# Kernel tuning notes

Measured on AMD Instinct MI355X. Metric: run time of the kernel, lower is better.

## Reference

```python
import jax, jax.numpy as jnp
import numpy as np

B, N, EMB, H, C = 1, 4096, 256, 4, 64  # heads*C == 256 feeds Linear(256, EMB)
NEG_SLOPE = 0.2
LN_EPS = 1e-5


def setup_inputs() -> dict:
    key = jax.random.key(0)
    ks = jax.random.split(key, 8)
    x = jax.random.normal(ks[0], (B, N, EMB), jnp.float32)
    adj = jax.random.randint(ks[1], (B, N, N), 0, 2, jnp.int32)
    W_lin = jax.random.normal(ks[2], (EMB, H * C), jnp.float32) * (1.0 / EMB) ** 0.5
    att_src = jax.random.normal(ks[3], (H, C), jnp.float32) * 0.1
    att_dst = jax.random.normal(ks[4], (H, C), jnp.float32) * 0.1
    bias_att = jax.random.normal(ks[5], (H * C,), jnp.float32) * 0.02
    W_out = jax.random.normal(ks[6], (H * C, EMB), jnp.float32) * (1.0 / (H * C)) ** 0.5
    b_out = jax.random.normal(ks[7], (EMB,), jnp.float32) * 0.02
    gamma = jnp.ones((EMB,), jnp.float32)
    beta = jnp.zeros((EMB,), jnp.float32)
    return dict(x=x, adj=adj, W_lin=W_lin, att_src=att_src, att_dst=att_dst,
                bias_att=bias_att, W_out=W_out, b_out=b_out, gamma=gamma, beta=beta)


def reference(x, adj, W_lin, att_src, att_dst, bias_att, W_out, b_out, gamma, beta):
    # DenseGATConv (concat=True, add_loop=True, negative_slope=0.2)
    h = (x @ W_lin).reshape(B, N, H, C)                       # [B,N,H,C]
    a_src = jnp.einsum('bnhc,hc->bnh', h, att_src)            # per source node j
    a_dst = jnp.einsum('bnhc,hc->bnh', h, att_dst)            # per dest node i
    # alpha[b,i,j,h] = a_src[b,j,h] + a_dst[b,i,h]
    alpha = a_src[:, None, :, :] + a_dst[:, :, None, :]       # [B,N,N,H]
    alpha = jnp.where(alpha >= 0, alpha, NEG_SLOPE * alpha)   # leaky_relu
    # add self-loops to adjacency, then mask and softmax over source axis j
    idx = jnp.arange(N)
    adj_sl = adj.at[:, idx, idx].set(1)
    alpha = jnp.where(adj_sl[..., None] == 0, -jnp.inf, alpha)
    alpha = jax.nn.softmax(alpha, axis=2)                     # [B,N,N,H]
    out = jnp.einsum('bijh,bjhc->bihc', alpha, h)             # aggregate sources
    out = out.reshape(B, N, H * C) + bias_att                 # concat heads + GAT bias
    # trailing Linear + LayerNorm
    y = out @ W_out + b_out                                   # [B,N,EMB]
    mu = jnp.mean(y, axis=-1, keepdims=True)
    var = jnp.mean((y - mu) ** 2, axis=-1, keepdims=True)
    return (y - mu) * jax.lax.rsqrt(var + LN_EPS) * gamma + beta
```

## Files before the change

kernel.cpp:

```cpp
#include <hip/hip_runtime.h>
#include <stdint.h>

#define N    4096
#define EMB  256
#define NH   4
#define HC   64
#define PAD  40

typedef __attribute__((ext_vector_type(8))) short s16x8;
typedef __attribute__((ext_vector_type(4))) short s16x4;
typedef __attribute__((ext_vector_type(4))) float f32x4;
typedef __attribute__((ext_vector_type(4))) int   i32x4;
typedef unsigned short ushort_t;

__device__ __forceinline__ unsigned short f2bf(float f) {
  unsigned int u = __builtin_bit_cast(unsigned int, f);
  u += 0x7fffu + ((u >> 16) & 1u);
  return (unsigned short)(u >> 16);
}

__global__ __launch_bounds__(256)
void k_prep(const float* __restrict__ W0, ushort_t* __restrict__ WP0,
            const float* __restrict__ W1, ushort_t* __restrict__ WP1,
            const int* __restrict__ adj, unsigned int* __restrict__ abits)
{
  int b = blockIdx.x;
  if (b < 4096) {
    const int i = b;
    const int t = threadIdx.x;
    const int* src = adj + (size_t)i * N + t * 16;
    i32x4 v0 = *(const i32x4*)(src);
    i32x4 v1 = *(const i32x4*)(src + 4);
    i32x4 v2 = *(const i32x4*)(src + 8);
    i32x4 v3 = *(const i32x4*)(src + 12);
    unsigned int m = 0;
    #pragma unroll
    for (int u = 0; u < 4; ++u) {
      m |= (v0[u] != 0 ? 1u : 0u) << u;
      m |= (v1[u] != 0 ? 1u : 0u) << (4 + u);
      m |= (v2[u] != 0 ? 1u : 0u) << (8 + u);
      m |= (v3[u] != 0 ? 1u : 0u) << (12 + u);
    }
    if ((i >> 4) == t) m |= 1u << (i & 15);
    unsigned int partner = __shfl_xor(m, 1);
    if ((t & 1) == 0) {
      unsigned int word = m | (partner << 16);
      abits[(size_t)(t >> 1) * N + i] = word;
    }
  } else {
    b -= 4096;
    int k = b & 255;
    int m = threadIdx.x;
    size_t dst = ((size_t)(k >> 5) * 256 + m) * 32 + (k & 31);
    if (b < 256) WP0[dst] = f2bf(W0[k * EMB + m]);
    else         WP1[dst] = f2bf(W1[k * EMB + m]);
  }
}

__global__ __launch_bounds__(256, 2)
void k1_gemm_h(const float* __restrict__ x,
               const ushort_t* __restrict__ WlP,
               const float* __restrict__ att_src,
               const float* __restrict__ att_dst,
               ushort_t* __restrict__ hS,
               float* __restrict__ a_srcT,
               float* __restrict__ a_dstT)
{
  __shared__ ushort_t T_lds[64][PAD];
  __shared__ float red_lds[2][2][32];
  const int t = threadIdx.x;
  const int lane = t & 63;
  const int w = t >> 6;
  const int ihalf = w & 1, chalf = w >> 1;
  const int i0 = blockIdx.x * 32;
  const int head = blockIdx.y;
  const int c0 = head * 64;
  const int lq = lane >> 4, lm = lane & 15;

  f32x4 acc[2];
  acc[0] = f32x4{0.f, 0.f, 0.f, 0.f};
  acc[1] = f32x4{0.f, 0.f, 0.f, 0.f};

  const float* xrow = x + (size_t)(i0 + ihalf * 16 + lm) * EMB + lq * 8;
  const ushort_t* wp0 = WlP + (size_t)(c0 + chalf * 32 + lm) * 32 + lq * 8;
  const ushort_t* wp1 = WlP + (size_t)(c0 + chalf * 32 + 16 + lm) * 32 + lq * 8;

  #pragma unroll 2
  for (int kp = 0; kp < 8; ++kp) {
    f32x4 v0 = *(const f32x4*)(xrow + kp * 32);
    f32x4 v1 = *(const f32x4*)(xrow + kp * 32 + 4);
    s16x8 a;
    a[0]=(short)f2bf(v0[0]); a[1]=(short)f2bf(v0[1]); a[2]=(short)f2bf(v0[2]); a[3]=(short)f2bf(v0[3]);
    a[4]=(short)f2bf(v1[0]); a[5]=(short)f2bf(v1[1]); a[6]=(short)f2bf(v1[2]); a[7]=(short)f2bf(v1[3]);
    s16x8 b0 = *(const s16x8*)(wp0 + (size_t)kp * 8192);
    s16x8 b1 = *(const s16x8*)(wp1 + (size_t)kp * 8192);
    acc[0] = __builtin_amdgcn_mfma_f32_16x16x32_bf16(a, b0, acc[0], 0, 0, 0);
    acc[1] = __builtin_amdgcn_mfma_f32_16x16x32_bf16(a, b1, acc[1], 0, 0, 0);
  }

  float ps[4] = {0.f,0.f,0.f,0.f}, pd[4] = {0.f,0.f,0.f,0.f};
  #pragma unroll
  for (int nf = 0; nf < 2; ++nf) {
    int c = chalf * 32 + nf * 16 + lm;
    float wsv = att_src[c0 + c];
    float wdv = att_dst[c0 + c];
    #pragma unroll
    for (int r = 0; r < 4; ++r) {
      float v = acc[nf][r];
      T_lds[c][ihalf * 16 + lq * 4 + r] = f2bf(v);
      ps[r] += v * wsv;
      pd[r] += v * wdv;
    }
  }
  #pragma unroll
  for (int r = 0; r < 4; ++r) {
    #pragma unroll
    for (int mm = 1; mm < 16; mm <<= 1) {
      ps[r] += __shfl_xor(ps[r], mm);
      pd[r] += __shfl_xor(pd[r], mm);
    }
  }
  if (lm == 0) {
    #pragma unroll
    for (int r = 0; r < 4; ++r) {
      int node = ihalf * 16 + lq * 4 + r;
      red_lds[0][chalf][node] = ps[r];
      red_lds[1][chalf][node] = pd[r];
    }
  }
  __syncthreads();
  if (t < 32) {
    a_srcT[head * N + i0 + t] = red_lds[0][0][t] + red_lds[0][1][t];
    a_dstT[head * N + i0 + t] = red_lds[1][0][t] + red_lds[1][1][t];
  }
  {
    int c = t >> 2, seg = t & 3;
    s16x8 v = *(const s16x8*)&T_lds[c][seg * 8];
    size_t base = (((size_t)head * 128 + (i0 >> 5)) * 64 + c) * 32 + seg * 8;
    *(s16x8*)(hS + base) = v;
  }
}

__global__ __launch_bounds__(512, 1)
void k34_attn(const unsigned int* __restrict__ abits,
              const ushort_t* __restrict__ hS,
              const float* __restrict__ a_srcT,
              const float* __restrict__ a_dstT,
              const float* __restrict__ bias_att,
              ushort_t* __restrict__ oS)
{
  __shared__ float acc_lds[2][3][32][65];
  __shared__ float l_lds[2][4][32];

  const int t = threadIdx.x;
  const int lane = t & 63;
  const int w = t >> 6;
  const int hloc = w & 1;
  const int jq = w >> 1;
  const int head = blockIdx.y * 2 + hloc;
  const int i0 = blockIdx.x * 32;
  const int lm = lane & 15, lq = lane >> 4;
  const int ig0 = i0 + lm;
  const int ig1 = i0 + 16 + lm;

  const float* asrc_h = a_srcT + head * N;
  const ushort_t* hS_h = hS + (size_t)head * 128 * 64 * 32;
  const float ad0 = a_dstT[head * N + ig0];
  const float ad1 = a_dstT[head * N + ig1];

  f32x4 acc[2][4];
  #pragma unroll
  for (int s = 0; s < 2; ++s)
    #pragma unroll
    for (int nf = 0; nf < 4; ++nf) acc[s][nf] = f32x4{0.f, 0.f, 0.f, 0.f};
  float lp0 = 0.f, lp1 = 0.f;

  #pragma unroll 2
  for (int it = 0; it < 32; ++it) {
    const int jw = jq * 32 + it;
    const int jl = jw * 32 + lq * 8;

    unsigned int word0 = abits[(size_t)jw * N + ig0];
    unsigned int word1 = abits[(size_t)jw * N + ig1];
    f32x4 as0 = *(const f32x4*)(asrc_h + jl);
    f32x4 as1 = *(const f32x4*)(asrc_h + jl + 4);

    const ushort_t* tile = hS_h + (size_t)jw * 2048;
    s16x8 b0 = *(const s16x8*)(tile + ( 0 + lm) * 32 + lq * 8);
    s16x8 b1 = *(const s16x8*)(tile + (16 + lm) * 32 + lq * 8);
    s16x8 b2 = *(const s16x8*)(tile + (32 + lm) * 32 + lq * 8);
    s16x8 b3 = *(const s16x8*)(tile + (48 + lm) * 32 + lq * 8);

    unsigned int e0[8], e1[8];
    #pragma unroll
    for (int jj = 0; jj < 8; ++jj) {
      float asv = (jj < 4) ? as0[jj] : as1[jj - 4];
      float sc0 = asv + ad0;
      float sc1 = asv + ad1;
      sc0 = fmaxf(sc0, 0.2f * sc0);
      sc1 = fmaxf(sc1, 0.2f * sc1);
      bool c0 = (word0 >> (lq * 8 + jj)) & 1u;
      bool c1 = (word1 >> (lq * 8 + jj)) & 1u;
      float v0 = c0 ? __expf(sc0) : 0.f;
      float v1 = c1 ? __expf(sc1) : 0.f;
      unsigned int eb0 = __builtin_bit_cast(unsigned int, v0) & 0xffff0000u;
      unsigned int eb1 = __builtin_bit_cast(unsigned int, v1) & 0xffff0000u;
      e0[jj] = eb0;
      e1[jj] = eb1;
      lp0 += __builtin_bit_cast(float, eb0);
      lp1 += __builtin_bit_cast(float, eb1);
    }
    i32x4 p0, p1;
    #pragma unroll
    for (int u = 0; u < 4; ++u) {
      p0[u] = (int)__builtin_amdgcn_perm(e0[2 * u + 1], e0[2 * u], 0x07060302u);
      p1[u] = (int)__builtin_amdgcn_perm(e1[2 * u + 1], e1[2 * u], 0x07060302u);
    }
    s16x8 af0 = __builtin_bit_cast(s16x8, p0);
    s16x8 af1 = __builtin_bit_cast(s16x8, p1);

    acc[0][0] = __builtin_amdgcn_mfma_f32_16x16x32_bf16(af0, b0, acc[0][0], 0, 0, 0);
    acc[0][1] = __builtin_amdgcn_mfma_f32_16x16x32_bf16(af0, b1, acc[0][1], 0, 0, 0);
    acc[0][2] = __builtin_amdgcn_mfma_f32_16x16x32_bf16(af0, b2, acc[0][2], 0, 0, 0);
    acc[0][3] = __builtin_amdgcn_mfma_f32_16x16x32_bf16(af0, b3, acc[0][3], 0, 0, 0);
    acc[1][0] = __builtin_amdgcn_mfma_f32_16x16x32_bf16(af1, b0, acc[1][0], 0, 0, 0);
    acc[1][1] = __builtin_amdgcn_mfma_f32_16x16x32_bf16(af1, b1, acc[1][1], 0, 0, 0);
    acc[1][2] = __builtin_amdgcn_mfma_f32_16x16x32_bf16(af1, b2, acc[1][2], 0, 0, 0);
    acc[1][3] = __builtin_amdgcn_mfma_f32_16x16x32_bf16(af1, b3, acc[1][3], 0, 0, 0);
  }

  lp0 += __shfl_xor(lp0, 16);
  lp0 += __shfl_xor(lp0, 32);
  lp1 += __shfl_xor(lp1, 16);
  lp1 += __shfl_xor(lp1, 32);
  if (lq == 0) {
    l_lds[hloc][jq][lm] = lp0;
    l_lds[hloc][jq][16 + lm] = lp1;
  }

  if (jq != 0) {
    #pragma unroll
    for (int s = 0; s < 2; ++s)
      #pragma unroll
      for (int nf = 0; nf < 4; ++nf)
        #pragma unroll
        for (int r = 0; r < 4; ++r)
          acc_lds[hloc][jq - 1][s * 16 + lq * 4 + r][nf * 16 + lm] = acc[s][nf][r];
  }
  __syncthreads();
  if (jq == 0) {
    #pragma unroll
    for (int s = 0; s < 2; ++s) {
      float linv[4];
      #pragma unroll
      for (int r = 0; r < 4; ++r) {
        int row = s * 16 + lq * 4 + r;
        linv[r] = 1.f / (l_lds[hloc][0][row] + l_lds[hloc][1][row] +
                         l_lds[hloc][2][row] + l_lds[hloc][3][row]);
      }
      #pragma unroll
      for (int nf = 0; nf < 4; ++nf) {
        float bia = bias_att[head * 64 + nf * 16 + lm];
        #pragma unroll
        for (int r = 0; r < 4; ++r) {
          int row = s * 16 + lq * 4 + r;
          float v = acc[s][nf][r] + acc_lds[hloc][0][row][nf * 16 + lm]
                                  + acc_lds[hloc][1][row][nf * 16 + lm]
                                  + acc_lds[hloc][2][row][nf * 16 + lm];
          size_t idx = (((size_t)((i0 >> 4) + s) * 8) + head * 2 + (nf >> 1)) * 512
                     + (lq * 4 + r) * 32 + (nf & 1) * 16 + lm;
          oS[idx] = f2bf(v * linv[r] + bia);
        }
      }
    }
  }
}

__global__ __launch_bounds__(256, 2)
void k5_gemm_ln(const ushort_t* __restrict__ oS,
                const ushort_t* __restrict__ WoP,
                const float* __restrict__ b_out,
                const float* __restrict__ gamma,
                const float* __restrict__ beta,
                float* __restrict__ out)
{
  __shared__ float y_lds[16][260];
  const int t = threadIdx.x, lane = t & 63, w = t >> 6;
  const int i0 = blockIdx.x * 16;
  const int lq = lane >> 4, lm = lane & 15;

  f32x4 acc[4];
  #pragma unroll
  for (int nf = 0; nf < 4; ++nf) acc[nf] = f32x4{0.f, 0.f, 0.f, 0.f};

  const ushort_t* oS_b = oS + (size_t)(i0 >> 4) * 4096 + lm * 32 + lq * 8;
  const ushort_t* wp0 = WoP + (size_t)(w * 64 +  0 + lm) * 32 + lq * 8;
  const ushort_t* wp1 = WoP + (size_t)(w * 64 + 16 + lm) * 32 + lq * 8;
  const ushort_t* wp2 = WoP + (size_t)(w * 64 + 32 + lm) * 32 + lq * 8;
  const ushort_t* wp3 = WoP + (size_t)(w * 64 + 48 + lm) * 32 + lq * 8;

  #pragma unroll 2
  for (int kp = 0; kp < 8; ++kp) {
    s16x8 a  = *(const s16x8*)(oS_b + (size_t)kp * 512);
    s16x8 b0 = *(const s16x8*)(wp0 + (size_t)kp * 8192);
    s16x8 b1 = *(const s16x8*)(wp1 + (size_t)kp * 8192);
    s16x8 b2 = *(const s16x8*)(wp2 + (size_t)kp * 8192);
    s16x8 b3 = *(const s16x8*)(wp3 + (size_t)kp * 8192);
    acc[0] = __builtin_amdgcn_mfma_f32_16x16x32_bf16(a, b0, acc[0], 0, 0, 0);
    acc[1] = __builtin_amdgcn_mfma_f32_16x16x32_bf16(a, b1, acc[1], 0, 0, 0);
    acc[2] = __builtin_amdgcn_mfma_f32_16x16x32_bf16(a, b2, acc[2], 0, 0, 0);
    acc[3] = __builtin_amdgcn_mfma_f32_16x16x32_bf16(a, b3, acc[3], 0, 0, 0);
  }
  #pragma unroll
  for (int nf = 0; nf < 4; ++nf)
    #pragma unroll
    for (int r = 0; r < 4; ++r) {
      int row = lq * 4 + r;
      int col = w * 64 + nf * 16 + lm;
      y_lds[row][col] = acc[nf][r] + b_out[col];
    }
  __syncthreads();
  f32x4 g  = *(const f32x4*)(gamma + lane * 4);
  f32x4 be = *(const f32x4*)(beta + lane * 4);
  #pragma unroll
  for (int r = w * 4; r < w * 4 + 4; ++r) {
    f32x4 v = *(const f32x4*)&y_lds[r][lane * 4];
    float s1 = v[0] + v[1] + v[2] + v[3];
    float s2 = v[0]*v[0] + v[1]*v[1] + v[2]*v[2] + v[3]*v[3];
    #pragma unroll
    for (int mm = 1; mm < 64; mm <<= 1) { s1 += __shfl_xor(s1, mm); s2 += __shfl_xor(s2, mm); }
    float mu = s1 * (1.f / 256.f);
    float var = s2 * (1.f / 256.f) - mu * mu;
    float rs = rsqrtf(var + 1e-5f);
    f32x4 o;
    #pragma unroll
    for (int u = 0; u < 4; ++u) o[u] = (v[u] - mu) * rs * g[u] + be[u];
    *(f32x4*)(out + (size_t)(i0 + r) * EMB + lane * 4) = o;
  }
}

extern "C" void kernel_launch(void* const* d_in, const int* in_sizes, int n_in,
                              void* d_out, int out_size, void* d_ws, size_t ws_size,
                              hipStream_t stream)
{
  (void)in_sizes; (void)n_in; (void)out_size; (void)ws_size;
  const float* x        = (const float*)d_in[0];
  const int*   adj      = (const int*)d_in[1];
  const float* W_lin    = (const float*)d_in[2];
  const float* att_src  = (const float*)d_in[3];
  const float* att_dst  = (const float*)d_in[4];
  const float* bias_att = (const float*)d_in[5];
  const float* W_out    = (const float*)d_in[6];
  const float* b_out    = (const float*)d_in[7];
  const float* gamma    = (const float*)d_in[8];
  const float* beta     = (const float*)d_in[9];
  float* out = (float*)d_out;

  uint8_t* p = (uint8_t*)d_ws;
  ushort_t* WlP = (ushort_t*)p;  p += (size_t)EMB * EMB * sizeof(ushort_t);
  ushort_t* WoP = (ushort_t*)p;  p += (size_t)EMB * EMB * sizeof(ushort_t);
  ushort_t* hS  = (ushort_t*)p;  p += (size_t)NH * HC * N * sizeof(ushort_t);
  float* a_srcb = (float*)p;     p += (size_t)NH * N * sizeof(float);
  float* a_dstb = (float*)p;     p += (size_t)NH * N * sizeof(float);
  ushort_t* oS  = (ushort_t*)p;  p += (size_t)N * EMB * sizeof(ushort_t);
  unsigned int* abits = (unsigned int*)p; p += (size_t)(N / 32) * N * sizeof(unsigned int);

  k_prep<<<4096 + 512, 256, 0, stream>>>(W_lin, WlP, W_out, WoP, adj, abits);
  k1_gemm_h<<<dim3(N / 32, NH), 256, 0, stream>>>(x, WlP, att_src, att_dst, hS, a_srcb, a_dstb);
  k34_attn<<<dim3(N / 32, 2), 512, 0, stream>>>(abits, hS, a_srcb, a_dstb, bias_att, oS);
  k5_gemm_ln<<<N / 16, 256, 0, stream>>>(oS, WoP, b_out, gamma, beta, out);
}
```

Before: 167.2 us.

## Split attention blocks per head with 8-way source split and two blocks per CU

Each attention block now handles a single head, with its eight waves splitting the source-node range eight ways instead of two heads with four-way splits. The grid doubles to N/32 x NH, and launch bounds ask for two blocks per CU to raise occupancy. The per-block reduction grows to seven LDS partial accumulators and an eight-term softmax denominator. This gives more blocks and latency hiding at the cost of more cross-wave reduction traffic and possible register pressure from the tighter bound.

```diff
diff --git a/kernel.cpp b/kernel.cpp
--- a/kernel.cpp
+++ b/kernel.cpp
@@ -141,7 +141,7 @@
   }
 }
 
-__global__ __launch_bounds__(512, 1)
+__global__ __launch_bounds__(512, 2)
 void k34_attn(const unsigned int* __restrict__ abits,
               const ushort_t* __restrict__ hS,
               const float* __restrict__ a_srcT,
@@ -149,15 +149,13 @@
               const float* __restrict__ bias_att,
               ushort_t* __restrict__ oS)
 {
-  __shared__ float acc_lds[2][3][32][65];
-  __shared__ float l_lds[2][4][32];
+  __shared__ float acc_lds[7][32][65];
+  __shared__ float l_lds[8][32];
 
   const int t = threadIdx.x;
   const int lane = t & 63;
-  const int w = t >> 6;
-  const int hloc = w & 1;
-  const int jq = w >> 1;
-  const int head = blockIdx.y * 2 + hloc;
+  const int jq = t >> 6;
+  const int head = blockIdx.y;
   const int i0 = blockIdx.x * 32;
   const int lm = lane & 15, lq = lane >> 4;
   const int ig0 = i0 + lm;
@@ -176,8 +174,8 @@
   float lp0 = 0.f, lp1 = 0.f;
 
   #pragma unroll 2
-  for (int it = 0; it < 32; ++it) {
-    const int jw = jq * 32 + it;
+  for (int it = 0; it < 16; ++it) {
+    const int jw = jq * 16 + it;
     const int jl = jw * 32 + lq * 8;
 
     unsigned int word0 = abits[(size_t)jw * N + ig0];
@@ -234,8 +232,8 @@
   lp1 += __shfl_xor(lp1, 16);
   lp1 += __shfl_xor(lp1, 32);
   if (lq == 0) {
-    l_lds[hloc][jq][lm] = lp0;
-    l_lds[hloc][jq][16 + lm] = lp1;
+    l_lds[jq][lm] = lp0;
+    l_lds[jq][16 + lm] = lp1;
   }
 
   if (jq != 0) {
@@ -245,7 +243,7 @@
       for (int nf = 0; nf < 4; ++nf)
         #pragma unroll
         for (int r = 0; r < 4; ++r)
-          acc_lds[hloc][jq - 1][s * 16 + lq * 4 + r][nf * 16 + lm] = acc[s][nf][r];
+          acc_lds[jq - 1][s * 16 + lq * 4 + r][nf * 16 + lm] = acc[s][nf][r];
   }
   __syncthreads();
   if (jq == 0) {
@@ -255,8 +253,10 @@
       #pragma unroll
       for (int r = 0; r < 4; ++r) {
         int row = s * 16 + lq * 4 + r;
-        linv[r] = 1.f / (l_lds[hloc][0][row] + l_lds[hloc][1][row] +
-                         l_lds[hloc][2][row] + l_lds[hloc][3][row]);
+        float sum = 0.f;
+        #pragma unroll
+        for (int q = 0; q < 8; ++q) sum += l_lds[q][row];
+        linv[r] = 1.f / sum;
       }
       #pragma unroll
       for (int nf = 0; nf < 4; ++nf) {
@@ -264,9 +264,9 @@
         #pragma unroll
         for (int r = 0; r < 4; ++r) {
           int row = s * 16 + lq * 4 + r;
-          float v = acc[s][nf][r] + acc_lds[hloc][0][row][nf * 16 + lm]
-                                  + acc_lds[hloc][1][row][nf * 16 + lm]
-                                  + acc_lds[hloc][2][row][nf * 16 + lm];
+          float v = acc[s][nf][r];
+          #pragma unroll
+          for (int q = 0; q < 7; ++q) v += acc_lds[q][row][nf * 16 + lm];
           size_t idx = (((size_t)((i0 >> 4) + s) * 8) + head * 2 + (nf >> 1)) * 512
                      + (lq * 4 + r) * 32 + (nf & 1) * 16 + lm;
           oS[idx] = f2bf(v * linv[r] + bia);
@@ -367,6 +367,6 @@
 
   k_prep<<<4096 + 512, 256, 0, stream>>>(W_lin, WlP, W_out, WoP, adj, abits);
   k1_gemm_h<<<dim3(N / 32, NH), 256, 0, stream>>>(x, WlP, att_src, att_dst, hS, a_srcb, a_dstb);
-  k34_attn<<<dim3(N / 32, 2), 512, 0, stream>>>(abits, hS, a_srcb, a_dstb, bias_att, oS);
+  k34_attn<<<dim3(N / 32, NH), 512, 0, stream>>>(abits, hS, a_srcb, a_dstb, bias_att, oS);
   k5_gemm_ln<<<N / 16, 256, 0, stream>>>(oS, WoP, b_out, gamma, beta, out);
 }
```

New measurement: 165.6 us. No clear change (-1.0%).
